# Kernel tuning notes

Hardware: AMD Instinct MI355X
Metric: run time of the kernel (lower is better)

## Reference

```python
import jax, jax.numpy as jnp
import numpy as np

N = 8192
IN_DIM = 512
OUT_DIM = 256
ALPHA = 0.2  # LeakyReLU negative slope


def setup_inputs() -> dict:
    key = jax.random.key(0)
    k_nodes, k_edge, k_W, k_Wb, k_a1, k_a1b, k_a2, k_a2b = jax.random.split(key, 8)
    nodes = jax.random.normal(k_nodes, (N, IN_DIM), dtype=jnp.float32)
    edge_mat = jax.random.uniform(k_edge, (N, N)) > 0.5
    edge_mat = edge_mat | jnp.eye(N, dtype=bool)
    s_W = 1.0 / np.sqrt(IN_DIM)
    s_a = 1.0 / np.sqrt(OUT_DIM)
    W_w = jax.random.uniform(k_W, (OUT_DIM, IN_DIM), minval=-s_W, maxval=s_W, dtype=jnp.float32)
    W_b = jax.random.uniform(k_Wb, (OUT_DIM,), minval=-s_W, maxval=s_W, dtype=jnp.float32)
    a1_w = jax.random.uniform(k_a1, (1, OUT_DIM), minval=-s_a, maxval=s_a, dtype=jnp.float32)
    a1_b = jax.random.uniform(k_a1b, (1,), minval=-s_a, maxval=s_a, dtype=jnp.float32)
    a2_w = jax.random.uniform(k_a2, (1, OUT_DIM), minval=-s_a, maxval=s_a, dtype=jnp.float32)
    a2_b = jax.random.uniform(k_a2b, (1,), minval=-s_a, maxval=s_a, dtype=jnp.float32)
    return {"nodes": nodes, "edge_mat": edge_mat, "W_w": W_w, "W_b": W_b,
            "a1_w": a1_w, "a1_b": a1_b, "a2_w": a2_w, "a2_b": a2_b}


def reference(nodes, edge_mat, W_w, W_b, a1_w, a1_b, a2_w, a2_b):
    Wh = nodes @ W_w.T + W_b                      # [N, OUT_DIM]
    Wh1 = Wh @ a1_w.T + a1_b                      # [N, 1]
    Wh2 = Wh @ a2_w.T + a2_b                      # [N, 1]
    scores = jax.nn.leaky_relu(Wh1 + Wh2.T, negative_slope=ALPHA)  # [N, N]
    masked = jnp.where(edge_mat, scores, -jnp.inf)
    attention = jax.nn.softmax(masked, axis=1)    # [N, N]
    return attention @ Wh                         # [N, OUT_DIM]
```

## Files before the change

kernel.cpp:

```cpp
#include <hip/hip_runtime.h>
#include <hip/hip_bf16.h>
#include <stdint.h>


#define NN 8192
#define IND 512
#define OUTD 256

typedef __attribute__((ext_vector_type(8))) short short8;
typedef __attribute__((ext_vector_type(4))) short short4v;
typedef __attribute__((ext_vector_type(4))) float f32x4;
typedef __attribute__((ext_vector_type(4))) unsigned int u32x4;

#define AS_GLOBAL __attribute__((address_space(1)))
#define AS_LDS __attribute__((address_space(3)))

static __device__ __forceinline__ short f2bf(float f) {
  return __builtin_bit_cast(short, __float2bfloat16(f));
}

extern "C" __global__ __launch_bounds__(256) void k_convert_w(
    const float* __restrict__ W, short* __restrict__ W2) {
  const int t = blockIdx.x * 256 + threadIdx.x;
  const int row = t >> 6, kb = t & 63;
  const float* src = W + row * IND + kb * 8;
  f32x4 x0 = *(const f32x4*)src;
  f32x4 x1 = *(const f32x4*)(src + 4);
  short8 o;
  o[0] = f2bf(x0[0]); o[1] = f2bf(x0[1]); o[2] = f2bf(x0[2]); o[3] = f2bf(x0[3]);
  o[4] = f2bf(x1[0]); o[5] = f2bf(x1[1]); o[6] = f2bf(x1[2]); o[7] = f2bf(x1[3]);
  *(short8*)(W2 + (size_t)kb * 2048 + row * 8) = o;
}

extern "C" __global__ __launch_bounds__(256, 2) void k_front(
    const int* __restrict__ mask, uint32_t* __restrict__ bm,
    const float* __restrict__ nodes, const short* __restrict__ W2,
    const float* __restrict__ Wb, const float* __restrict__ a1w,
    const float* __restrict__ a1b, const float* __restrict__ a2w,
    const float* __restrict__ a2b, short* __restrict__ WhL,
    float* __restrict__ s1, float* __restrict__ sAC,
    uint32_t* __restrict__ sPK) {
  const int bid = blockIdx.x;
  const int tid = threadIdx.x;
  const int wv = tid >> 6, lane = tid & 63;

  if (bid % 9 != 8) {
    const int mb = (bid / 9) * 8 + (bid % 9);
    const int gw = mb * 4 + wv;
    const size_t base = (size_t)gw * 16384;
#pragma unroll 4
    for (int it = 0; it < 64; ++it) {
      const size_t ib = base + (size_t)it * 256;
      unsigned long long b0 = __ballot(mask[ib + lane] != 0);
      unsigned long long b1 = __ballot(mask[ib + 64 + lane] != 0);
      unsigned long long b2 = __ballot(mask[ib + 128 + lane] != 0);
      unsigned long long b3 = __ballot(mask[ib + 192 + lane] != 0);
      if (lane < 8) {
        unsigned long long s01 = (lane & 2) ? b1 : b0;
        unsigned long long s23 = (lane & 2) ? b3 : b2;
        unsigned long long sel = (lane & 4) ? s23 : s01;
        bm[ib / 32 + lane] = (uint32_t)(sel >> ((lane & 1) * 32));
      }
    }
    return;
  }

  const int wb = bid / 9;
  const int g = lane >> 4, m = lane & 15;
  const int rowbase = wb * 64 + wv * 16;

  f32x4 acc[16];
#pragma unroll
  for (int nf = 0; nf < 16; ++nf) acc[nf] = (f32x4){0.f, 0.f, 0.f, 0.f};

  const float* arow = nodes + (size_t)(rowbase + m) * IND;
  const short* bb = W2 + (size_t)g * 2048 + m * 8;
#pragma unroll 4
  for (int k0 = 0; k0 < IND; k0 += 32) {
    const float* ap = arow + k0 + g * 8;
    f32x4 x0 = *(const f32x4*)ap;
    f32x4 x1 = *(const f32x4*)(ap + 4);
    short8 af;
    af[0] = f2bf(x0[0]); af[1] = f2bf(x0[1]); af[2] = f2bf(x0[2]); af[3] = f2bf(x0[3]);
    af[4] = f2bf(x1[0]); af[5] = f2bf(x1[1]); af[6] = f2bf(x1[2]); af[7] = f2bf(x1[3]);
    const short* bk = bb + (size_t)(k0 >> 3) * 2048;
#pragma unroll
    for (int nf = 0; nf < 16; ++nf) {
      short8 bf = *(const short8*)(bk + nf * 128);
      acc[nf] = __builtin_amdgcn_mfma_f32_16x16x32_bf16(af, bf, acc[nf], 0, 0, 0);
    }
  }

  float p1[4] = {0.f, 0.f, 0.f, 0.f}, p2[4] = {0.f, 0.f, 0.f, 0.f};
#pragma unroll
  for (int nf = 0; nf < 16; ++nf) {
    const int n = nf * 16 + m;
    const float b = Wb[n], c1 = a1w[n], c2 = a2w[n];
#pragma unroll
    for (int r = 0; r < 4; ++r) {
      float v = acc[nf][r] + b;
      acc[nf][r] = v;
      p1[r] += c1 * v;
      p2[r] += c2 * v;
    }
  }
#pragma unroll
  for (int off = 1; off < 16; off <<= 1) {
#pragma unroll
    for (int r = 0; r < 4; ++r) {
      p1[r] += __shfl_xor(p1[r], off);
      p2[r] += __shfl_xor(p2[r], off);
    }
  }
  if (m == 0) {
    const float b1 = a1b[0], b2 = a2b[0];
#pragma unroll
    for (int r = 0; r < 4; ++r) {
      const int row = rowbase + g * 4 + r;
      const float v1 = p1[r] + b1, v2 = p2[r] + b2;
      s1[row] = v1;
      sAC[row] = __expf(v1);
      sAC[NN + row] = __expf(0.2f * v1);
      const float B = __expf(v2), D = __expf(0.2f * v2);
      sPK[2 * row] = __builtin_bit_cast(uint32_t, B);
      sPK[2 * row + 1] =
          ((uint32_t)(uint16_t)f2bf(D) << 16) | (uint16_t)f2bf(v2);
    }
  }

  const size_t cbase = ((size_t)(rowbase >> 3) + (g >> 1)) * 2048 + (g & 1) * 4;
#pragma unroll
  for (int nf = 0; nf < 16; ++nf) {
    short4v o;
#pragma unroll
    for (int r = 0; r < 4; ++r) o[r] = f2bf(acc[nf][r]);
    *(short4v*)(WhL + cbase + (size_t)(nf * 16 + m) * 8) = o;
  }
}

extern "C" __global__ __launch_bounds__(512, 4) void k_attn(
    const uint32_t* __restrict__ bm, const short* __restrict__ WhL,
    const float* __restrict__ s1, const float* __restrict__ sAC,
    const uint32_t* __restrict__ sPK,
    float* __restrict__ pnum, float* __restrict__ pden) {
  __shared__ char smem[73728];
  uint32_t* PKs = (uint32_t*)(smem + 49152);
  uint32_t* BMs = (uint32_t*)(smem + 57344);

  const int tid = threadIdx.x;
  const int w = tid >> 6, lane = tid & 63, g = lane >> 4, m = lane & 15;
  const int rt = blockIdx.x >> 3, jc = blockIdx.x & 7;
  const int rg = w & 3, ns = w >> 2;
  const int rb = rt * 128 + rg * 32;

  const float T0 = -s1[rb + m],        T1 = -s1[rb + 16 + m];
  const float A0 = sAC[rb + m],        A1 = sAC[rb + 16 + m];
  const float C0 = sAC[NN + rb + m],   C1 = sAC[NN + rb + 16 + m];

  f32x4 acc0[8], acc1[8];
#pragma unroll
  for (int nf = 0; nf < 8; ++nf) {
    acc0[nf] = (f32x4){0.f, 0.f, 0.f, 0.f};
    acc1[nf] = (f32x4){0.f, 0.f, 0.f, 0.f};
  }
  float den0 = 0.f, den1 = 0.f;

  {
    const int rloc = tid >> 2, wq = (tid & 3) * 8;
    const uint32_t* src = bm + (size_t)(rt * 128 + rloc) * 256 + jc * 32 + wq;
    u32x4 a = *(const u32x4*)src;
    u32x4 b = *(const u32x4*)(src + 4);
#pragma unroll
    for (int i = 0; i < 4; ++i)
      BMs[rloc * 32 + ((wq + i) ^ (rloc & 31))] = a[i];
#pragma unroll
    for (int i = 0; i < 4; ++i)
      BMs[rloc * 32 + ((wq + 4 + i) ^ (rloc & 31))] = b[i];
  }
  __builtin_amdgcn_global_load_lds(
      (const AS_GLOBAL void*)((const char*)sPK + (size_t)jc * 8192 +
                              w * 1024 + lane * 16),
      (AS_LDS void*)(smem + 49152 + w * 1024), 16, 0, 0);
  const short* gS = WhL + (size_t)jc * 262144;
#pragma unroll
  for (int s = 0; s < 2; ++s) {
#pragma unroll
    for (int c = 0; c < 2; ++c) {
      __builtin_amdgcn_global_load_lds(
          (const AS_GLOBAL void*)(gS + s * 8192 + w * 1024 + c * 512 + lane * 8),
          (AS_LDS void*)(smem + s * 16384 + w * 2048 + c * 1024), 16, 0, 0);
    }
  }
  __syncthreads();

  auto build = [&](float T, float A, float C, uint32_t mbits,
                   const u32x4& q0, const u32x4& q1,
                   const u32x4& q2, const u32x4& q3, float& den) -> short8 {
    const uint32_t Bv[8] = {q0[0], q0[2], q1[0], q1[2],
                            q2[0], q2[2], q3[0], q3[2]};
    const uint32_t Dv[8] = {q0[1], q0[3], q1[1], q1[3],
                            q2[1], q2[3], q3[1], q3[3]};
    short8 af;
#pragma unroll
    for (int i = 0; i < 8; ++i) {
      const float s2v = __builtin_bit_cast(float, Dv[i] << 16);
      const bool pos = s2v > T;
      const float wv = __builtin_bit_cast(float, pos ? Bv[i] : (Dv[i] & 0xFFFF0000u));
      const float a = pos ? A : C;
      const float val = wv * a;
      const float pv = ((mbits >> i) & 1u) ? val : 0.f;
      den += pv;
      af[i] = f2bf(pv);
    }
    return af;
  };

  for (int u = 0; u < 32; ++u) {
    asm volatile("s_waitcnt vmcnt(2)" ::: "memory");
    __builtin_amdgcn_s_barrier();
    __builtin_amdgcn_sched_barrier(0);

    {
      const int up = (u + 2 < 32) ? (u + 2) : 31;
      const int bi = (u + 2) % 3;
      const short* gn = gS + up * 8192 + w * 1024 + lane * 8;
      char* ldb = smem + bi * 16384 + w * 2048;
      __builtin_amdgcn_global_load_lds((const AS_GLOBAL void*)gn,
                                       (AS_LDS void*)ldb, 16, 0, 0);
      __builtin_amdgcn_global_load_lds((const AS_GLOBAL void*)(gn + 512),
                                       (AS_LDS void*)(ldb + 1024), 16, 0, 0);
    }

    const uint32_t cw0 = BMs[(rg * 32 + m) * 32 + (u ^ m)];
    const uint32_t cw1 = BMs[(rg * 32 + 16 + m) * 32 + (u ^ (16 + m))];
    const uint32_t* pk = &PKs[u * 64 + g * 16];
    const u32x4 q0 = *(const u32x4*)(pk + 0);
    const u32x4 q1 = *(const u32x4*)(pk + 4);
    const u32x4 q2 = *(const u32x4*)(pk + 8);
    const u32x4 q3 = *(const u32x4*)(pk + 12);
    short8 af0 = build(T0, A0, C0, cw0 >> (g * 8), q0, q1, q2, q3, den0);
    short8 af1 = build(T1, A1, C1, cw1 >> (g * 8), q0, q1, q2, q3, den1);

    const short* bl = (const short*)(smem + (u % 3) * 16384) +
                      g * 2048 + (ns * 128 + m) * 8;
#pragma unroll
    for (int nf = 0; nf < 8; ++nf) {
      short8 bf = *(const short8*)(bl + nf * 128);
      acc0[nf] = __builtin_amdgcn_mfma_f32_16x16x32_bf16(af0, bf, acc0[nf], 0, 0, 0);
      acc1[nf] = __builtin_amdgcn_mfma_f32_16x16x32_bf16(af1, bf, acc1[nf], 0, 0, 0);
    }
  }

  den0 += __shfl_xor(den0, 16); den0 += __shfl_xor(den0, 32);
  den1 += __shfl_xor(den1, 16); den1 += __shfl_xor(den1, 32);
  if (ns == 0 && lane < 16) {
    pden[jc * NN + rb + m] = den0;
    pden[jc * NN + rb + 16 + m] = den1;
  }

  float* pn = pnum + (size_t)jc * NN * OUTD + (size_t)rb * OUTD + ns * 128;
#pragma unroll
  for (int r = 0; r < 4; ++r) {
    const int q = g * 4 + r;
#pragma unroll
    for (int nf = 0; nf < 8; ++nf) {
      pn[(size_t)q * OUTD + nf * 16 + m] = acc0[nf][r];
      pn[(size_t)(16 + q) * OUTD + nf * 16 + m] = acc1[nf][r];
    }
  }
}

extern "C" __global__ __launch_bounds__(256) void k_comb(
    const float* __restrict__ pnum, const float* __restrict__ pden,
    float* __restrict__ out) {
  const int idx = blockIdx.x * 256 + threadIdx.x;
  const int row = idx >> 6, c4 = (idx & 63) * 4;
  f32x4 s = (f32x4){0.f, 0.f, 0.f, 0.f};
  float d = 0.f;
#pragma unroll
  for (int jc = 0; jc < 8; ++jc) {
    f32x4 v = *(const f32x4*)(pnum + ((size_t)jc * NN + row) * OUTD + c4);
    s += v;
    d += pden[jc * NN + row];
  }
  const float inv = 1.f / d;
  *(f32x4*)(out + (size_t)row * OUTD + c4) = s * inv;
}

extern "C" void kernel_launch(void* const* d_in, const int* in_sizes, int n_in,
                              void* d_out, int out_size, void* d_ws, size_t ws_size,
                              hipStream_t stream) {
  const float* nodes = (const float*)d_in[0];
  const int*   mask  = (const int*)d_in[1];
  const float* W_w   = (const float*)d_in[2];
  const float* W_b   = (const float*)d_in[3];
  const float* a1w   = (const float*)d_in[4];
  const float* a1b   = (const float*)d_in[5];
  const float* a2w   = (const float*)d_in[6];
  const float* a2b   = (const float*)d_in[7];
  float* out = (float*)d_out;

  char* ws = (char*)d_ws;
  short*    WhL  = (short*)(ws);
  float*    s1   = (float*)(ws + (size_t)4  * 1024 * 1024);
  short*    W2   = (short*)(ws + (size_t)4  * 1024 * 1024 + 65536);
  uint32_t* bmp  = (uint32_t*)(ws + (size_t)5  * 1024 * 1024);
  float*    sAC  = (float*)(ws + (size_t)13 * 1024 * 1024);
  uint32_t* sPK  = (uint32_t*)(ws + (size_t)14 * 1024 * 1024);
  float*    pnum = (float*)(ws + (size_t)16 * 1024 * 1024);
  float*    pden = (float*)(ws + (size_t)96 * 1024 * 1024);

  hipLaunchKernelGGL(k_convert_w, dim3(64), dim3(256), 0, stream, W_w, W2);
  hipLaunchKernelGGL(k_front, dim3(1152), dim3(256), 0, stream,
                     mask, bmp, nodes, W2, W_b, a1w, a1b, a2w, a2b,
                     WhL, s1, sAC, sPK);
  hipLaunchKernelGGL(k_attn, dim3(512), dim3(512), 0, stream,
                     bmp, WhL, s1, sAC, sPK, pnum, pden);
  hipLaunchKernelGGL(k_comb, dim3(2048), dim3(256), 0, stream,
                     pnum, pden, out);
}
```

Measured before the change: 176.5 us.

## Halve attention rows per block, pack score terms into bf16 pairs, raise occupancy

After: 180.2 us. 2.1% more time.

```diff
diff --git a/kernel.cpp b/kernel.cpp
--- a/kernel.cpp
+++ b/kernel.cpp
@@ -38,8 +38,7 @@
     const float* __restrict__ Wb, const float* __restrict__ a1w,
     const float* __restrict__ a1b, const float* __restrict__ a2w,
     const float* __restrict__ a2b, short* __restrict__ WhL,
-    float* __restrict__ s1, float* __restrict__ sAC,
-    uint32_t* __restrict__ sPK) {
+    float* __restrict__ sAC, uint32_t* __restrict__ sPK) {
   const int bid = blockIdx.x;
   const int tid = threadIdx.x;
   const int wv = tid >> 6, lane = tid & 63;
@@ -118,13 +117,11 @@
     for (int r = 0; r < 4; ++r) {
       const int row = rowbase + g * 4 + r;
       const float v1 = p1[r] + b1, v2 = p2[r] + b2;
-      s1[row] = v1;
       sAC[row] = __expf(v1);
       sAC[NN + row] = __expf(0.2f * v1);
+      sAC[2 * NN + row] = __expf(-0.2f * v1);
       const float B = __expf(v2), D = __expf(0.2f * v2);
-      sPK[2 * row] = __builtin_bit_cast(uint32_t, B);
-      sPK[2 * row + 1] =
-          ((uint32_t)(uint16_t)f2bf(D) << 16) | (uint16_t)f2bf(v2);
+      sPK[row] = ((uint32_t)(uint16_t)f2bf(B) << 16) | (uint16_t)f2bf(D);
     }
   }
 
@@ -138,76 +135,59 @@
   }
 }
 
-extern "C" __global__ __launch_bounds__(512, 4) void k_attn(
+extern "C" __global__ __launch_bounds__(512, 6) void k_attn(
     const uint32_t* __restrict__ bm, const short* __restrict__ WhL,
-    const float* __restrict__ s1, const float* __restrict__ sAC,
-    const uint32_t* __restrict__ sPK,
+    const float* __restrict__ sAC, const uint32_t* __restrict__ sPK,
     float* __restrict__ pnum, float* __restrict__ pden) {
-  __shared__ char smem[73728];
+  __shared__ char smem[53248];
   uint32_t* PKs = (uint32_t*)(smem + 49152);
-  uint32_t* BMs = (uint32_t*)(smem + 57344);
 
   const int tid = threadIdx.x;
   const int w = tid >> 6, lane = tid & 63, g = lane >> 4, m = lane & 15;
   const int rt = blockIdx.x >> 3, jc = blockIdx.x & 7;
   const int rg = w & 3, ns = w >> 2;
-  const int rb = rt * 128 + rg * 32;
-
-  const float T0 = -s1[rb + m],        T1 = -s1[rb + 16 + m];
-  const float A0 = sAC[rb + m],        A1 = sAC[rb + 16 + m];
-  const float C0 = sAC[NN + rb + m],   C1 = sAC[NN + rb + 16 + m];
-
-  f32x4 acc0[8], acc1[8];
-#pragma unroll
-  for (int nf = 0; nf < 8; ++nf) {
-    acc0[nf] = (f32x4){0.f, 0.f, 0.f, 0.f};
-    acc1[nf] = (f32x4){0.f, 0.f, 0.f, 0.f};
-  }
-  float den0 = 0.f, den1 = 0.f;
-
-  {
-    const int rloc = tid >> 2, wq = (tid & 3) * 8;
-    const uint32_t* src = bm + (size_t)(rt * 128 + rloc) * 256 + jc * 32 + wq;
-    u32x4 a = *(const u32x4*)src;
-    u32x4 b = *(const u32x4*)(src + 4);
-#pragma unroll
-    for (int i = 0; i < 4; ++i)
-      BMs[rloc * 32 + ((wq + i) ^ (rloc & 31))] = a[i];
-#pragma unroll
-    for (int i = 0; i < 4; ++i)
-      BMs[rloc * 32 + ((wq + 4 + i) ^ (rloc & 31))] = b[i];
-  }
-  __builtin_amdgcn_global_load_lds(
-      (const AS_GLOBAL void*)((const char*)sPK + (size_t)jc * 8192 +
-                              w * 1024 + lane * 16),
-      (AS_LDS void*)(smem + 49152 + w * 1024), 16, 0, 0);
+  const int rb = rt * 64 + rg * 16;
+
+  const float A0   = sAC[rb + m];
+  const float C0   = sAC[NN + rb + m];
+  const float invC = sAC[2 * NN + rb + m];
+
+  f32x4 acc[8];
+#pragma unroll
+  for (int nf = 0; nf < 8; ++nf) acc[nf] = (f32x4){0.f, 0.f, 0.f, 0.f};
+  float den = 0.f;
+
+  const uint32_t* bw = bm + (size_t)(rb + m) * 256 + jc * 32;
   const short* gS = WhL + (size_t)jc * 262144;
+
+  uint32_t cwA = bw[0];
+  uint32_t cwB = bw[1];
+  if (tid < 256) {
+    __builtin_amdgcn_global_load_lds(
+        (const AS_GLOBAL void*)((const char*)sPK + (size_t)jc * 4096 + tid * 16),
+        (AS_LDS void*)(smem + 49152 + tid * 16), 16, 0, 0);
+  }
 #pragma unroll
   for (int s = 0; s < 2; ++s) {
-#pragma unroll
-    for (int c = 0; c < 2; ++c) {
-      __builtin_amdgcn_global_load_lds(
-          (const AS_GLOBAL void*)(gS + s * 8192 + w * 1024 + c * 512 + lane * 8),
-          (AS_LDS void*)(smem + s * 16384 + w * 2048 + c * 1024), 16, 0, 0);
-    }
-  }
-  __syncthreads();
-
-  auto build = [&](float T, float A, float C, uint32_t mbits,
-                   const u32x4& q0, const u32x4& q1,
-                   const u32x4& q2, const u32x4& q3, float& den) -> short8 {
-    const uint32_t Bv[8] = {q0[0], q0[2], q1[0], q1[2],
-                            q2[0], q2[2], q3[0], q3[2]};
-    const uint32_t Dv[8] = {q0[1], q0[3], q1[1], q1[3],
-                            q2[1], q2[3], q3[1], q3[3]};
+    const short* gsl = gS + s * 8192 + tid * 8;
+    char* dst = smem + s * 16384 + tid * 16;
+    __builtin_amdgcn_global_load_lds((const AS_GLOBAL void*)gsl,
+                                     (AS_LDS void*)dst, 16, 0, 0);
+    __builtin_amdgcn_global_load_lds((const AS_GLOBAL void*)(gsl + 4096),
+                                     (AS_LDS void*)(dst + 8192), 16, 0, 0);
+  }
+  asm volatile("s_waitcnt vmcnt(0)" ::: "memory");
+  __builtin_amdgcn_s_barrier();
+
+  auto build = [&](uint32_t mbits, const u32x4& q0, const u32x4& q1) -> short8 {
     short8 af;
 #pragma unroll
     for (int i = 0; i < 8; ++i) {
-      const float s2v = __builtin_bit_cast(float, Dv[i] << 16);
-      const bool pos = s2v > T;
-      const float wv = __builtin_bit_cast(float, pos ? Bv[i] : (Dv[i] & 0xFFFF0000u));
-      const float a = pos ? A : C;
-      const float val = wv * a;
+      const uint32_t pw = (i < 4) ? q0[i] : q1[i - 4];
+      const float D = __builtin_bit_cast(float, pw << 16);
+      const float B = __builtin_bit_cast(float, pw & 0xFFFF0000u);
+      const bool pos = D > invC;
+      const float val = pos ? B * A0 : D * C0;
       const float pv = ((mbits >> i) & 1u) ? val : 0.f;
       den += pv;
       af[i] = f2bf(pv);
@@ -215,48 +195,47 @@
     return af;
   };
 
-  for (int u = 0; u < 32; ++u) {
-    asm volatile("s_waitcnt vmcnt(2)" ::: "memory");
+  auto body = [&](int u, uint32_t& cw) {
+    asm volatile("s_waitcnt vmcnt(3)" ::: "memory");
     __builtin_amdgcn_s_barrier();
     __builtin_amdgcn_sched_barrier(0);
-
     {
-      const int up = (u + 2 < 32) ? (u + 2) : 31;
+      const int up = (u + 2 < 32) ? u + 2 : 31;
       const int bi = (u + 2) % 3;
-      const short* gn = gS + up * 8192 + w * 1024 + lane * 8;
-      char* ldb = smem + bi * 16384 + w * 2048;
+      const short* gn = gS + up * 8192 + tid * 8;
+      char* dst = smem + bi * 16384 + tid * 16;
       __builtin_amdgcn_global_load_lds((const AS_GLOBAL void*)gn,
-                                       (AS_LDS void*)ldb, 16, 0, 0);
-      __builtin_amdgcn_global_load_lds((const AS_GLOBAL void*)(gn + 512),
-                                       (AS_LDS void*)(ldb + 1024), 16, 0, 0);
-    }
-
-    const uint32_t cw0 = BMs[(rg * 32 + m) * 32 + (u ^ m)];
-    const uint32_t cw1 = BMs[(rg * 32 + 16 + m) * 32 + (u ^ (16 + m))];
-    const uint32_t* pk = &PKs[u * 64 + g * 16];
+                                       (AS_LDS void*)dst, 16, 0, 0);
+      __builtin_amdgcn_global_load_lds((const AS_GLOBAL void*)(gn + 4096),
+                                       (AS_LDS void*)(dst + 8192), 16, 0, 0);
+    }
+    const uint32_t* pk = &PKs[u * 32 + g * 8];
     const u32x4 q0 = *(const u32x4*)(pk + 0);
     const u32x4 q1 = *(const u32x4*)(pk + 4);
-    const u32x4 q2 = *(const u32x4*)(pk + 8);
-    const u32x4 q3 = *(const u32x4*)(pk + 12);
-    short8 af0 = build(T0, A0, C0, cw0 >> (g * 8), q0, q1, q2, q3, den0);
-    short8 af1 = build(T1, A1, C1, cw1 >> (g * 8), q0, q1, q2, q3, den1);
-
+    short8 af = build(cw >> (g * 8), q0, q1);
     const short* bl = (const short*)(smem + (u % 3) * 16384) +
                       g * 2048 + (ns * 128 + m) * 8;
+    __builtin_amdgcn_s_setprio(1);
 #pragma unroll
     for (int nf = 0; nf < 8; ++nf) {
       short8 bf = *(const short8*)(bl + nf * 128);
-      acc0[nf] = __builtin_amdgcn_mfma_f32_16x16x32_bf16(af0, bf, acc0[nf], 0, 0, 0);
-      acc1[nf] = __builtin_amdgcn_mfma_f32_16x16x32_bf16(af1, bf, acc1[nf], 0, 0, 0);
-    }
-  }
-
-  den0 += __shfl_xor(den0, 16); den0 += __shfl_xor(den0, 32);
-  den1 += __shfl_xor(den1, 16); den1 += __shfl_xor(den1, 32);
-  if (ns == 0 && lane < 16) {
-    pden[jc * NN + rb + m] = den0;
-    pden[jc * NN + rb + 16 + m] = den1;
-  }
+      acc[nf] = __builtin_amdgcn_mfma_f32_16x16x32_bf16(af, bf, acc[nf], 0, 0, 0);
+    }
+    __builtin_amdgcn_s_setprio(0);
+    {
+      const int ub = (u + 2 < 32) ? u + 2 : 31;
+      cw = bw[ub];
+    }
+  };
+
+  for (int uu = 0; uu < 32; uu += 2) {
+    body(uu, cwA);
+    body(uu + 1, cwB);
+  }
+
+  den += __shfl_xor(den, 16);
+  den += __shfl_xor(den, 32);
+  if (ns == 0 && lane < 16) pden[jc * NN + rb + m] = den;
 
   float* pn = pnum + (size_t)jc * NN * OUTD + (size_t)rb * OUTD + ns * 128;
 #pragma unroll
@@ -264,8 +243,7 @@
     const int q = g * 4 + r;
 #pragma unroll
     for (int nf = 0; nf < 8; ++nf) {
-      pn[(size_t)q * OUTD + nf * 16 + m] = acc0[nf][r];
-      pn[(size_t)(16 + q) * OUTD + nf * 16 + m] = acc1[nf][r];
+      pn[(size_t)q * OUTD + nf * 16 + m] = acc[nf][r];
     }
   }
 }
@@ -302,7 +280,6 @@
 
   char* ws = (char*)d_ws;
   short*    WhL  = (short*)(ws);
-  float*    s1   = (float*)(ws + (size_t)4  * 1024 * 1024);
   short*    W2   = (short*)(ws + (size_t)4  * 1024 * 1024 + 65536);
   uint32_t* bmp  = (uint32_t*)(ws + (size_t)5  * 1024 * 1024);
   float*    sAC  = (float*)(ws + (size_t)13 * 1024 * 1024);
@@ -313,9 +290,9 @@
   hipLaunchKernelGGL(k_convert_w, dim3(64), dim3(256), 0, stream, W_w, W2);
   hipLaunchKernelGGL(k_front, dim3(1152), dim3(256), 0, stream,
                      mask, bmp, nodes, W2, W_b, a1w, a1b, a2w, a2b,
-                     WhL, s1, sAC, sPK);
-  hipLaunchKernelGGL(k_attn, dim3(512), dim3(512), 0, stream,
-                     bmp, WhL, s1, sAC, sPK, pnum, pden);
+                     WhL, sAC, sPK);
+  hipLaunchKernelGGL(k_attn, dim3(1024), dim3(512), 0, stream,
+                     bmp, WhL, sAC, sPK, pnum, pden);
   hipLaunchKernelGGL(k_comb, dim3(2048), dim3(256), 0, stream,
                      pnum, pden, out);
 }
```
